# Performance work log

Measured on AMD Instinct MI355X. Metric: run time of the kernel, lower is better.

Reference implementation:

```python
import jax, jax.numpy as jnp
import numpy as np

# --- constants from init_kwargs (inference mode: max_voxels[1]) ---
VOXEL_SIZE = np.array([0.16, 0.16, 4.0], np.float32)
PC_RANGE = np.array([0.0, -39.68, -3.0, 69.12, 39.68, 1.0], np.float32)
MAX_PTS = 32
MAX_VOX = 40000  # training=False -> max_voxels[1]
GRID = np.round((PC_RANGE[3:] - PC_RANGE[:3]) / VOXEL_SIZE).astype(np.int64)
NX, NY, NZ = int(GRID[0]), int(GRID[1]), int(GRID[2])  # 432, 496, 1
SENTINEL = NX * NY * NZ  # linear id for out-of-range points


def setup_inputs() -> dict:
    key = jax.random.key(0)
    N, C = 1_200_000, 5
    k1, k2 = jax.random.split(key)
    lo = jnp.asarray(PC_RANGE[:3])
    hi = jnp.asarray(PC_RANGE[3:])
    span = hi - lo
    xyz = jax.random.uniform(k1, (N, 3), dtype=jnp.float32) * span * 1.05 + lo - 0.025 * span
    feats = jax.random.normal(k2, (N, C), dtype=jnp.float32)
    return {"points_feats": jnp.concatenate([xyz, feats], axis=1)}


def reference(points_feats):
    """PointPillars voxelization.

    Returns fixed-shape (padded to MAX_VOX) versions of:
      out_voxels     [MAX_VOX, MAX_PTS, 3+C]  point coords+feats per voxel (0-padded)
      out_coords     [MAX_VOX, 3]             integer voxel coords in (z, y, x) order
      out_num_points [MAX_VOX]                number of points kept per voxel
    Voxels are ordered by linearized voxel id; points within a voxel keep
    their original order; at most MAX_PTS points per voxel, MAX_VOX voxels.
    """
    N = points_feats.shape[0]
    xyz = points_feats[:, :3]
    lo = jnp.asarray(PC_RANGE[:3])
    vs = jnp.asarray(VOXEL_SIZE)
    coords = jnp.floor((xyz - lo) / vs).astype(jnp.int32)  # [N,3] (x,y,z) voxel coords
    grid = jnp.array([NX, NY, NZ], jnp.int32)
    valid = jnp.all((coords >= 0) & (coords < grid), axis=1)
    vid = (coords[:, 2] * NY + coords[:, 1]) * NX + coords[:, 0]  # linear voxel id
    vid = jnp.where(valid, vid, SENTINEL)

    order = jnp.argsort(vid)            # stable: preserves point order within voxel
    svid = vid[order]
    valid_s = svid < SENTINEL
    new = jnp.concatenate([jnp.array([True]), svid[1:] != svid[:-1]]) & valid_s
    rank = jnp.cumsum(new.astype(jnp.int32)) - 1          # voxel index per point
    idx = jnp.arange(N, dtype=jnp.int32)
    pos = idx - jax.lax.cummax(jnp.where(new, idx, 0))    # slot within voxel

    keep = valid_s & (pos < MAX_PTS) & (rank < MAX_VOX)
    row = jnp.where(keep, rank, MAX_VOX)                  # dropped points -> dummy row
    col = jnp.where(keep, pos, 0)

    # dense point-index buffer; 0 means "empty slot" (matches feats zero-row trick)
    dense_idx = jnp.zeros((MAX_VOX + 1, MAX_PTS), jnp.int32)
    dense_idx = dense_idx.at[row, col].set(order.astype(jnp.int32) + 1)[:MAX_VOX]

    feats_pad = jnp.concatenate([jnp.zeros_like(points_feats[:1]), points_feats], axis=0)
    out_voxels = feats_pad[dense_idx]                     # [MAX_VOX, MAX_PTS, 3+C]

    # decode voxel coords (z, y, x) for the first point of each voxel
    vx = svid % NX
    vy = (svid // NX) % NY
    vz = svid // (NX * NY)
    zyx = jnp.stack([vz, vy, vx], axis=1).astype(jnp.int32)
    vrow = jnp.where(new & (rank < MAX_VOX), rank, MAX_VOX)
    out_coords = jnp.zeros((MAX_VOX + 1, 3), jnp.int32).at[vrow].set(zyx)[:MAX_VOX]

    out_num_points = jax.ops.segment_sum(
        keep.astype(jnp.int32), row, num_segments=MAX_VOX + 1)[:MAX_VOX]
    return out_voxels, out_coords, out_num_points
```

## Files before the change

kernel.cpp:

```cpp
#include <hip/hip_runtime.h>


constexpr int NXv = 432;
constexpr int NYv = 496;
constexpr int NZv = 1;
constexpr int NVOX = NXv * NYv * NZv;
constexpr int MAX_PTSv = 32;
constexpr int MAX_VOXv = 40000;
constexpr int SLOT_CAP = 64;
constexpr int SCAN_BS = 256;
constexpr int NBLK = NVOX / SCAN_BS;

constexpr size_t VOX_F   = (size_t)MAX_VOXv * MAX_PTSv * 8;
constexpr size_t COORD_F = (size_t)MAX_VOXv * 3;

__device__ __forceinline__ int voxel_id(float x, float y, float z) {
    float fx = x * 6.25f;
    float fy = (y + 39.68f) * 6.25f;
    float fz = (z + 3.0f) * 0.25f;
    int cx = (int)floorf(fx);
    int cy = (int)floorf(fy);
    int cz = (int)floorf(fz);
    if (cx < 0 || cx >= NXv || cy < 0 || cy >= NYv || cz < 0 || cz >= NZv)
        return -1;
    return (cz * NYv + cy) * NXv + cx;
}

__global__ void k_zero(unsigned int* p, int n) {
    int i = blockIdx.x * blockDim.x + threadIdx.x;
    int stride = gridDim.x * blockDim.x;
    for (; i < n; i += stride) p[i] = 0u;
}


__global__ void k_prep(const float* __restrict__ pf, int N,
                       int* __restrict__ vids, unsigned char* __restrict__ occ) {
    int i = blockIdx.x * blockDim.x + threadIdx.x;
    if (i >= N) return;
    float4 v = reinterpret_cast<const float4*>(pf)[(size_t)i * 2];
    int vid = voxel_id(v.x, v.y, v.z);
    vids[i] = vid;
    if (vid >= 0) occ[vid] = 1;
}

__global__ void k_blocksum2(const unsigned char* __restrict__ occ,
                            unsigned int* __restrict__ bsums) {
    int i = blockIdx.x * SCAN_BS + threadIdx.x;
    int flag = (occ[i] != 0) ? 1 : 0;
    unsigned long long b = __ballot(flag);
    __shared__ unsigned int wsum[SCAN_BS / 64];
    if ((threadIdx.x & 63) == 0) wsum[threadIdx.x >> 6] = (unsigned)__popcll(b);
    __syncthreads();
    if (threadIdx.x == 0) {
        unsigned s = 0;
        for (int w = 0; w < SCAN_BS / 64; ++w) s += wsum[w];
        bsums[blockIdx.x] = s;
    }
}

__global__ void k_ranks2(const unsigned char* __restrict__ occ,
                         const unsigned int* __restrict__ bsums,
                         int* __restrict__ rank_of, int* __restrict__ vid_of_rank) {
    int i = blockIdx.x * SCAN_BS + threadIdx.x;
    int t = threadIdx.x;
    int flag = (occ[i] != 0) ? 1 : 0;
    __shared__ unsigned int sh[SCAN_BS];
    sh[t] = (unsigned)flag;
    __syncthreads();
    for (int off = 1; off < SCAN_BS; off <<= 1) {
        unsigned add = (t >= off) ? sh[t - off] : 0u;
        __syncthreads();
        sh[t] += add;
        __syncthreads();
    }
    unsigned rank = bsums[blockIdx.x] + sh[t] - (unsigned)flag;
    int r = (flag && rank < (unsigned)MAX_VOXv) ? (int)rank : -1;
    rank_of[i] = r;
    if (r >= 0) vid_of_rank[r] = i;
}

__global__ void k_append2(const int* __restrict__ vids, int N,
                          const int* __restrict__ rank_of,
                          unsigned int* __restrict__ appcnt,
                          float* __restrict__ out) {
    int i = blockIdx.x * blockDim.x + threadIdx.x;
    if (i >= N) return;
    int vid = vids[i];
    if (vid < 0) return;
    int r = rank_of[vid];
    if (r < 0) return;
    unsigned s = atomicAdd(&appcnt[r], 1u);
    if (s < (unsigned)SLOT_CAP) {
        int* rowi = reinterpret_cast<int*>(out + (size_t)r * (MAX_PTSv * 8));
        rowi[s] = i;
    }
}


__global__ void k_count(const float* __restrict__ pf, int N,
                        unsigned int* __restrict__ counts) {
    int i = blockIdx.x * blockDim.x + threadIdx.x;
    if (i >= N) return;
    float4 v = reinterpret_cast<const float4*>(pf)[(size_t)i * 2];
    int vid = voxel_id(v.x, v.y, v.z);
    if (vid >= 0) atomicAdd(&counts[vid], 1u);
}

__global__ void k_blocksum(const unsigned int* __restrict__ counts,
                           unsigned int* __restrict__ bsums) {
    int i = blockIdx.x * SCAN_BS + threadIdx.x;
    int flag = (counts[i] != 0u) ? 1 : 0;
    unsigned long long b = __ballot(flag);
    __shared__ unsigned int wsum[SCAN_BS / 64];
    if ((threadIdx.x & 63) == 0) wsum[threadIdx.x >> 6] = (unsigned)__popcll(b);
    __syncthreads();
    if (threadIdx.x == 0) {
        unsigned s = 0;
        for (int w = 0; w < SCAN_BS / 64; ++w) s += wsum[w];
        bsums[blockIdx.x] = s;
    }
}

__global__ void k_ranks(const unsigned int* __restrict__ counts,
                        const unsigned int* __restrict__ bsums,
                        int* __restrict__ rank_of, int* __restrict__ vid_of_rank) {
    int i = blockIdx.x * SCAN_BS + threadIdx.x;
    int t = threadIdx.x;
    int flag = (counts[i] != 0u) ? 1 : 0;
    __shared__ unsigned int sh[SCAN_BS];
    sh[t] = (unsigned)flag;
    __syncthreads();
    for (int off = 1; off < SCAN_BS; off <<= 1) {
        unsigned add = (t >= off) ? sh[t - off] : 0u;
        __syncthreads();
        sh[t] += add;
        __syncthreads();
    }
    unsigned rank = bsums[blockIdx.x] + sh[t] - (unsigned)flag;
    int r = (flag && rank < (unsigned)MAX_VOXv) ? (int)rank : -1;
    rank_of[i] = r;
    if (r >= 0) vid_of_rank[r] = i;
}

__global__ void k_append(const float* __restrict__ pf, int N,
                         const int* __restrict__ rank_of,
                         unsigned int* __restrict__ appcnt,
                         float* __restrict__ out) {
    int i = blockIdx.x * blockDim.x + threadIdx.x;
    if (i >= N) return;
    float4 v = reinterpret_cast<const float4*>(pf)[(size_t)i * 2];
    int vid = voxel_id(v.x, v.y, v.z);
    if (vid < 0) return;
    int r = rank_of[vid];
    if (r < 0) return;
    unsigned s = atomicAdd(&appcnt[r], 1u);
    if (s < (unsigned)SLOT_CAP) {
        int* rowi = reinterpret_cast<int*>(out + (size_t)r * (MAX_PTSv * 8));
        rowi[s] = i;
    }
}


__global__ void k_scan_bsums(unsigned int* __restrict__ bsums,
                             unsigned int* __restrict__ scal) {
    __shared__ unsigned int sh[1024];
    int t = threadIdx.x;
    unsigned v = (t < NBLK) ? bsums[t] : 0u;
    sh[t] = v;
    __syncthreads();
    for (int off = 1; off < 1024; off <<= 1) {
        unsigned add = (t >= off) ? sh[t - off] : 0u;
        __syncthreads();
        sh[t] += add;
        __syncthreads();
    }
    if (t < NBLK) bsums[t] = sh[t] - v;
    if (t == NBLK - 1) scal[0] = sh[t];
}

__global__ void k_emit(const float* __restrict__ pf,
                       const unsigned int* __restrict__ appcnt,
                       const int* __restrict__ vid_of_rank,
                       const unsigned int* __restrict__ scal,
                       float* __restrict__ out) {
    int r = blockIdx.x;
    int t = threadIdx.x;
    float* row       = out + (size_t)r * (MAX_PTSv * 8);
    float* out_coord = out + VOX_F;
    float* out_num   = out + VOX_F + COORD_F;
    unsigned K = min(scal[0], (unsigned)MAX_VOXv);

    if ((unsigned)r >= K) {
        reinterpret_cast<float4*>(row)[t] = make_float4(0.f, 0.f, 0.f, 0.f);
        if (t == 0) {
            out_coord[(size_t)r * 3 + 0] = 0.f;
            out_coord[(size_t)r * 3 + 1] = 0.f;
            out_coord[(size_t)r * 3 + 2] = 0.f;
            out_num[r] = 0.f;
        }
        return;
    }

    __shared__ int sidx[SLOT_CAP];
    int c = (int)min(appcnt[r], (unsigned)SLOT_CAP);
    const int* rowi = reinterpret_cast<const int*>(row);
    sidx[t] = (t < c) ? rowi[t] : 0x7fffffff;
    __syncthreads();
    int nkeep = c < MAX_PTSv ? c : MAX_PTSv;

    if (t < c) {
        int my = sidx[t];
        int pos = 0;
        for (int j = 0; j < c; ++j) pos += (sidx[j] < my) ? 1 : 0;
        if (pos < MAX_PTSv) {
            const float4* src = reinterpret_cast<const float4*>(pf) + (size_t)my * 2;
            float4 a = src[0];
            float4 b = src[1];
            float4* dst = reinterpret_cast<float4*>(row + pos * 8);
            dst[0] = a;
            dst[1] = b;
        }
    }
    if (t >= nkeep && t < MAX_PTSv) {
        float4* dst = reinterpret_cast<float4*>(row + t * 8);
        dst[0] = make_float4(0.f, 0.f, 0.f, 0.f);
        dst[1] = make_float4(0.f, 0.f, 0.f, 0.f);
    }
    if (t == 0) {
        int vid = vid_of_rank[r];
        int vx = vid % NXv;
        int vy = (vid / NXv) % NYv;
        int vz = vid / (NXv * NYv);
        out_coord[(size_t)r * 3 + 0] = (float)vz;
        out_coord[(size_t)r * 3 + 1] = (float)vy;
        out_coord[(size_t)r * 3 + 2] = (float)vx;
        out_num[r] = (float)nkeep;
    }
}

extern "C" void kernel_launch(void* const* d_in, const int* in_sizes, int n_in,
                              void* d_out, int out_size, void* d_ws, size_t ws_size,
                              hipStream_t stream) {
    const float* pf = (const float*)d_in[0];
    const int N = in_sizes[0] / 8;
    float* out = (float*)d_out;

    const size_t OCC_B   = 215040;
    const size_t APP_B   = (size_t)MAX_VOXv * 4;
    const size_t BS_B    = 4096;
    const size_t SCAL_B  = 16;
    const size_t ZERO_B  = OCC_B + APP_B + BS_B + SCAL_B;
    const size_t RANK_B  = (size_t)NVOX * 4;
    const size_t VOR_B   = (size_t)MAX_VOXv * 4;
    const size_t NEED    = ZERO_B + RANK_B + VOR_B + (size_t)N * 4;

    char* wsb = (char*)d_ws;
    unsigned char* occ        = (unsigned char*)wsb;
    unsigned int* appcnt      = (unsigned int*)(wsb + OCC_B);
    unsigned int* bsums       = (unsigned int*)(wsb + OCC_B + APP_B);
    unsigned int* scal        = (unsigned int*)(wsb + OCC_B + APP_B + BS_B);
    int*          rank_of     = (int*)(wsb + ZERO_B);
    int*          vid_of_rank = (int*)(wsb + ZERO_B + RANK_B);
    int*          vids        = (int*)(wsb + ZERO_B + RANK_B + VOR_B);

    if (ws_size >= NEED) {
        k_zero<<<512, 256, 0, stream>>>((unsigned int*)wsb, (int)(ZERO_B / 4));
        k_prep<<<(N + 255) / 256, 256, 0, stream>>>(pf, N, vids, occ);
        k_blocksum2<<<NBLK, SCAN_BS, 0, stream>>>(occ, bsums);
        k_scan_bsums<<<1, 1024, 0, stream>>>(bsums, scal);
        k_ranks2<<<NBLK, SCAN_BS, 0, stream>>>(occ, bsums, rank_of, vid_of_rank);
        k_append2<<<(N + 255) / 256, 256, 0, stream>>>(vids, N, rank_of, appcnt, out);
        k_emit<<<MAX_VOXv, 64, 0, stream>>>(pf, appcnt, vid_of_rank, scal, out);
        return;
    }

    unsigned int* wsp          = (unsigned int*)d_ws;
    unsigned int* counts_f     = wsp;
    unsigned int* appcnt_f     = counts_f + NVOX;
    unsigned int* bsums_f      = appcnt_f + MAX_VOXv;
    unsigned int* scal_f       = bsums_f + 1024;
    int*          rank_of_f    = (int*)(scal_f + 4);
    int*          vid_of_rk_f  = rank_of_f + NVOX;

    const int n_zero = NVOX + MAX_VOXv + 1024 + 4;
    k_zero<<<512, 256, 0, stream>>>(wsp, n_zero);
    k_count<<<(N + 255) / 256, 256, 0, stream>>>(pf, N, counts_f);
    k_blocksum<<<NBLK, SCAN_BS, 0, stream>>>(counts_f, bsums_f);
    k_scan_bsums<<<1, 1024, 0, stream>>>(bsums_f, scal_f);
    k_ranks<<<NBLK, SCAN_BS, 0, stream>>>(counts_f, bsums_f, rank_of_f, vid_of_rk_f);
    k_append<<<(N + 255) / 256, 256, 0, stream>>>(pf, N, rank_of_f, appcnt_f, out);
    k_emit<<<MAX_VOXv, 64, 0, stream>>>(pf, appcnt_f, vid_of_rk_f, scal_f, out);
}
```

Before: 55.43 us.

## Replace three-kernel occupancy scan with single-pass decoupled look-back scan

Merges the block-sum, block-sums scan and rank kernels into one kernel that uses a decoupled look-back prefix scan over per-block status flags. This removes two kernel launches and a second pass over the occupancy array. The cost is spin-waiting on global atomics. Correctness depends on blocks being scheduled in forward order; 837 blocks should fit on the device at once, so deadlock is unlikely.

```diff
diff --git a/kernel.cpp b/kernel.cpp
--- a/kernel.cpp
+++ b/kernel.cpp
@@ -43,28 +43,17 @@
     if (vid >= 0) occ[vid] = 1;
 }
 
-__global__ void k_blocksum2(const unsigned char* __restrict__ occ,
-                            unsigned int* __restrict__ bsums) {
-    int i = blockIdx.x * SCAN_BS + threadIdx.x;
-    int flag = (occ[i] != 0) ? 1 : 0;
-    unsigned long long b = __ballot(flag);
-    __shared__ unsigned int wsum[SCAN_BS / 64];
-    if ((threadIdx.x & 63) == 0) wsum[threadIdx.x >> 6] = (unsigned)__popcll(b);
-    __syncthreads();
-    if (threadIdx.x == 0) {
-        unsigned s = 0;
-        for (int w = 0; w < SCAN_BS / 64; ++w) s += wsum[w];
-        bsums[blockIdx.x] = s;
-    }
-}
-
-__global__ void k_ranks2(const unsigned char* __restrict__ occ,
-                         const unsigned int* __restrict__ bsums,
-                         int* __restrict__ rank_of, int* __restrict__ vid_of_rank) {
-    int i = blockIdx.x * SCAN_BS + threadIdx.x;
+__global__ void k_scanranks(const unsigned char* __restrict__ occ,
+                            unsigned int* __restrict__ flags,
+                            unsigned int* __restrict__ scal,
+                            int* __restrict__ rank_of,
+                            int* __restrict__ vid_of_rank) {
+    int bid = blockIdx.x;
     int t = threadIdx.x;
+    int i = bid * SCAN_BS + t;
     int flag = (occ[i] != 0) ? 1 : 0;
     __shared__ unsigned int sh[SCAN_BS];
+    __shared__ unsigned int sh_excl;
     sh[t] = (unsigned)flag;
     __syncthreads();
     for (int off = 1; off < SCAN_BS; off <<= 1) {
@@ -73,10 +62,51 @@
         sh[t] += add;
         __syncthreads();
     }
-    unsigned rank = bsums[blockIdx.x] + sh[t] - (unsigned)flag;
+    unsigned total = sh[SCAN_BS - 1];
+
+    if (t == 0) {
+        unsigned st = (bid == 0) ? 2u : 1u;
+        atomicExch(&flags[bid], (st << 30) | total);
+        if (bid == 0) sh_excl = 0;
+    }
+
+    if (bid > 0 && t < 64) {
+        unsigned acc = 0;
+        int base = bid - 1;
+        int lane = t;
+        for (;;) {
+            int j = base - lane;
+            unsigned v;
+            if (j >= 0) {
+                do { v = atomicOr(&flags[j], 0u); } while ((v >> 30) == 0u);
+            } else {
+                v = (2u << 30);
+            }
+            unsigned st  = v >> 30;
+            unsigned val = v & 0x3FFFFFFFu;
+            unsigned long long b2 = __ballot(st == 2u);
+            int lstar = (b2 != 0ULL) ? (__ffsll((unsigned long long)b2) - 1) : 64;
+            unsigned contrib = (lane <= lstar) ? val : 0u;
+            #pragma unroll
+            for (int off = 32; off >= 1; off >>= 1)
+                contrib += __shfl_down(contrib, off);
+            if (lane == 0) acc += contrib;
+            if (lstar != 64) break;
+            base -= 64;
+        }
+        if (lane == 0) {
+            atomicExch(&flags[bid], (2u << 30) | (acc + total));
+            sh_excl = acc;
+        }
+    }
+    __syncthreads();
+    unsigned excl = sh_excl;
+
+    unsigned rank = excl + sh[t] - (unsigned)flag;
     int r = (flag && rank < (unsigned)MAX_VOXv) ? (int)rank : -1;
     rank_of[i] = r;
     if (r >= 0) vid_of_rank[r] = i;
+    if (bid == NBLK - 1 && t == 0) scal[0] = excl + total;
 }
 
 __global__ void k_append2(const int* __restrict__ vids, int N,
@@ -119,6 +149,23 @@
         for (int w = 0; w < SCAN_BS / 64; ++w) s += wsum[w];
         bsums[blockIdx.x] = s;
     }
+}
+
+__global__ void k_scan_bsums(unsigned int* __restrict__ bsums,
+                             unsigned int* __restrict__ scal) {
+    __shared__ unsigned int sh[1024];
+    int t = threadIdx.x;
+    unsigned v = (t < NBLK) ? bsums[t] : 0u;
+    sh[t] = v;
+    __syncthreads();
+    for (int off = 1; off < 1024; off <<= 1) {
+        unsigned add = (t >= off) ? sh[t - off] : 0u;
+        __syncthreads();
+        sh[t] += add;
+        __syncthreads();
+    }
+    if (t < NBLK) bsums[t] = sh[t] - v;
+    if (t == NBLK - 1) scal[0] = sh[t];
 }
 
 __global__ void k_ranks(const unsigned int* __restrict__ counts,
@@ -160,23 +207,6 @@
     }
 }
 
-
-__global__ void k_scan_bsums(unsigned int* __restrict__ bsums,
-                             unsigned int* __restrict__ scal) {
-    __shared__ unsigned int sh[1024];
-    int t = threadIdx.x;
-    unsigned v = (t < NBLK) ? bsums[t] : 0u;
-    sh[t] = v;
-    __syncthreads();
-    for (int off = 1; off < 1024; off <<= 1) {
-        unsigned add = (t >= off) ? sh[t - off] : 0u;
-        __syncthreads();
-        sh[t] += add;
-        __syncthreads();
-    }
-    if (t < NBLK) bsums[t] = sh[t] - v;
-    if (t == NBLK - 1) scal[0] = sh[t];
-}
 
 __global__ void k_emit(const float* __restrict__ pf,
                        const unsigned int* __restrict__ appcnt,
@@ -247,9 +277,9 @@
 
     const size_t OCC_B   = 215040;
     const size_t APP_B   = (size_t)MAX_VOXv * 4;
-    const size_t BS_B    = 4096;
-    const size_t SCAL_B  = 16;
-    const size_t ZERO_B  = OCC_B + APP_B + BS_B + SCAL_B;
+    const size_t FLAG_B  = 4096;
+    const size_t SCAL_B  = 64;
+    const size_t ZERO_B  = OCC_B + APP_B + FLAG_B + SCAL_B;
     const size_t RANK_B  = (size_t)NVOX * 4;
     const size_t VOR_B   = (size_t)MAX_VOXv * 4;
     const size_t NEED    = ZERO_B + RANK_B + VOR_B + (size_t)N * 4;
@@ -257,8 +287,8 @@
     char* wsb = (char*)d_ws;
     unsigned char* occ        = (unsigned char*)wsb;
     unsigned int* appcnt      = (unsigned int*)(wsb + OCC_B);
-    unsigned int* bsums       = (unsigned int*)(wsb + OCC_B + APP_B);
-    unsigned int* scal        = (unsigned int*)(wsb + OCC_B + APP_B + BS_B);
+    unsigned int* flags       = (unsigned int*)(wsb + OCC_B + APP_B);
+    unsigned int* scal        = (unsigned int*)(wsb + OCC_B + APP_B + FLAG_B);
     int*          rank_of     = (int*)(wsb + ZERO_B);
     int*          vid_of_rank = (int*)(wsb + ZERO_B + RANK_B);
     int*          vids        = (int*)(wsb + ZERO_B + RANK_B + VOR_B);
@@ -266,9 +296,7 @@
     if (ws_size >= NEED) {
         k_zero<<<512, 256, 0, stream>>>((unsigned int*)wsb, (int)(ZERO_B / 4));
         k_prep<<<(N + 255) / 256, 256, 0, stream>>>(pf, N, vids, occ);
-        k_blocksum2<<<NBLK, SCAN_BS, 0, stream>>>(occ, bsums);
-        k_scan_bsums<<<1, 1024, 0, stream>>>(bsums, scal);
-        k_ranks2<<<NBLK, SCAN_BS, 0, stream>>>(occ, bsums, rank_of, vid_of_rank);
+        k_scanranks<<<NBLK, SCAN_BS, 0, stream>>>(occ, flags, scal, rank_of, vid_of_rank);
         k_append2<<<(N + 255) / 256, 256, 0, stream>>>(vids, N, rank_of, appcnt, out);
         k_emit<<<MAX_VOXv, 64, 0, stream>>>(pf, appcnt, vid_of_rank, scal, out);
         return;
```

Result: slower. 57.16 us (+3.1%).
